# Performance work log

Hardware: AMD Instinct MI355X
Metric: run time of the kernel (lower is better)

The kernel has to match this reference:

```python
import jax, jax.numpy as jnp
import numpy as np

H = 4096
W = 4096
C = 3
OUT = 1024
MAX_MIP = 8  # matches init max_mip_level; mip chain is levels 0..MAX_MIP


def setup_inputs() -> dict:
    key = jax.random.key(0)
    k1, k2, k3 = jax.random.split(key, 3)
    data = jax.random.uniform(k1, (1, H, W, C), dtype=jnp.float32)
    texc = jax.random.uniform(k2, (1, OUT, OUT, 2), dtype=jnp.float32)
    # small UV derivatives -> per-pixel texel footprint of a few texels, so the
    # LOD spans several mip levels (exercises cross-level paged gathers)
    texc_deriv = jax.random.normal(k3, (1, OUT, OUT, 4), dtype=jnp.float32) * 2e-3
    return {"data": data, "texc": texc, "texc_deriv": texc_deriv}


def _avg_pool2(x):
    # 2x2 box-filter mipmap reduction, matching virtual_texture_mipmap_fwd
    b, h, w, c = x.shape
    return x.reshape(b, h // 2, 2, w // 2, 2, c).mean(axis=(2, 4))


def _bilinear_wrap(tex, texc):
    # tex: [1,h,w,c]; texc: [1,Ho,Wo,2] in [0,1); boundary_mode='wrap'
    h, w = tex.shape[1], tex.shape[2]
    x = texc[..., 0] * w - 0.5
    y = texc[..., 1] * h - 0.5
    x0f = jnp.floor(x)
    y0f = jnp.floor(y)
    fx = (x - x0f)[..., None]
    fy = (y - y0f)[..., None]
    x0 = x0f.astype(jnp.int32) % w
    y0 = y0f.astype(jnp.int32) % h
    x1 = (x0 + 1) % w
    y1 = (y0 + 1) % h
    t = tex[0]  # [h,w,c]
    top = t[y0, x0] * (1.0 - fx) + t[y0, x1] * fx
    bot = t[y1, x0] * (1.0 - fx) + t[y1, x1] * fx
    return top * (1.0 - fy) + bot * fy  # [1,Ho,Wo,c]


def _forward(data, texc, texc_deriv):
    # LOD from screen-space UV derivatives (nvdiffrast linear-mipmap-linear)
    dudx = texc_deriv[..., 0] * W
    dvdx = texc_deriv[..., 1] * H
    dudy = texc_deriv[..., 2] * W
    dvdy = texc_deriv[..., 3] * H
    rho2 = jnp.maximum(dudx * dudx + dvdx * dvdx, dudy * dudy + dvdy * dvdy)
    lod = 0.5 * jnp.log2(jnp.maximum(rho2, 1e-20))
    lod = jnp.clip(lod, 0.0, float(MAX_MIP))  # [1,Ho,Wo]

    # build mip pyramid (gradients flow back to base texture, matching
    # virtual_texture_mipmap_bwd accumulation)
    mips = [data]
    for _ in range(MAX_MIP):
        mips.append(_avg_pool2(mips[-1]))

    # trilinear: per-level weight w_l = clip(1 - |lod - l|, 0, 1)
    out = jnp.zeros(texc.shape[:-1] + (C,), dtype=data.dtype)
    for lvl in range(MAX_MIP + 1):
        w_l = jnp.clip(1.0 - jnp.abs(lod - float(lvl)), 0.0, 1.0)[..., None]
        out = out + w_l * _bilinear_wrap(mips[lvl], texc)
    return out


def reference(data, texc, texc_deriv):
    return _forward(data, texc, texc_deriv)
```

## Files before the change

kernel.cpp:

```cpp
#include <hip/hip_runtime.h>
#include <hip/hip_bf16.h>


#define OUT_N (1024 * 1024)

__device__ __forceinline__ unsigned mip_off_b(int lvl) {
    return (67108864u - (67108864u >> (2 * lvl - 2))) / 3u;
}
#define OFF6 22347776u

__device__ __forceinline__ unsigned pack10(float r, float g, float b) {
    unsigned ur = __float2uint_rn(r * 1023.0f);
    unsigned ug = __float2uint_rn(g * 1023.0f);
    unsigned ub = __float2uint_rn(b * 1023.0f);
    return ur | (ug << 10) | (ub << 20);
}

__device__ __forceinline__ void dec_acc(unsigned q, float w, float& r, float& g, float& b) {
    const float s = 1.0f / 1023.0f;
    r = fmaf((float)(q & 1023u) * s, w, r);
    g = fmaf((float)((q >> 10) & 1023u) * s, w, g);
    b = fmaf((float)((q >> 20) & 1023u) * s, w, b);
}

__device__ __forceinline__ float4 dec4(unsigned q) {
    const float s = 1.0f / 1023.0f;
    return float4{(float)(q & 1023u) * s, (float)((q >> 10) & 1023u) * s,
                  (float)((q >> 20) & 1023u) * s, 0.0f};
}

__device__ __forceinline__ float4 avg4(float4 a, float4 b, float4 c, float4 d) {
    return float4{(a.x + b.x + c.x + d.x) * 0.25f,
                  (a.y + b.y + c.y + d.y) * 0.25f,
                  (a.z + b.z + c.z + d.z) * 0.25f, 0.0f};
}

__device__ __forceinline__ void store_quad(char* p, float4 t00, float4 t01,
                                           float4 t10, float4 t11) {
    *(uint4*)p = make_uint4(pack10(t00.x, t00.y, t00.z), pack10(t01.x, t01.y, t01.z),
                            pack10(t10.x, t10.y, t10.z), pack10(t11.x, t11.y, t11.z));
}

__global__ __launch_bounds__(256) void mip_fused(const float* __restrict__ data,
                                                 char* __restrict__ wsb) {
    __shared__ float4 s1[32][33];
    __shared__ float4 s2[16][17];
    __shared__ float4 s3[8][9];
    __shared__ float4 s4[4][5];

    const int t = threadIdx.x;
    const int bx = blockIdx.x & 63;
    const int by = blockIdx.x >> 6;

    {
        int qx = t & 15, qy = t >> 4;
        int r0 = (by << 6) + (qy << 2);
        int c0 = (bx << 6) + (qx << 2);
        const float* p = data + ((size_t)r0 * 4096 + c0) * 3;
        float4 t00 = {0, 0, 0, 0}, t01 = {0, 0, 0, 0};
        float4 t10 = {0, 0, 0, 0}, t11 = {0, 0, 0, 0};
#pragma unroll
        for (int i = 0; i < 4; ++i) {
            const float4* rp = (const float4*)(p + (size_t)i * 4096 * 3);
            float4 A = rp[0], B = rp[1], C = rp[2];
            float ex = A.x + A.w, ey = A.y + B.x, ez = A.z + B.y;
            float fx_ = B.z + C.y, fy_ = B.w + C.z, fz_ = C.x + C.w;
            if (i < 2) {
                t00.x += ex; t00.y += ey; t00.z += ez;
                t01.x += fx_; t01.y += fy_; t01.z += fz_;
            } else {
                t10.x += ex; t10.y += ey; t10.z += ez;
                t11.x += fx_; t11.y += fy_; t11.z += fz_;
            }
        }
        t00.x *= 0.25f; t00.y *= 0.25f; t00.z *= 0.25f;
        t01.x *= 0.25f; t01.y *= 0.25f; t01.z *= 0.25f;
        t10.x *= 0.25f; t10.y *= 0.25f; t10.z *= 0.25f;
        t11.x *= 0.25f; t11.y *= 0.25f; t11.z *= 0.25f;
        s1[2 * qy][2 * qx] = t00;     s1[2 * qy][2 * qx + 1] = t01;
        s1[2 * qy + 1][2 * qx] = t10; s1[2 * qy + 1][2 * qx + 1] = t11;
    }
    __syncthreads();

    if (t < 64) {
        int qx = t & 7, qy = t >> 3;
        int sy = qy << 2, sx = qx << 2;
        float4 t00 = avg4(s1[sy][sx], s1[sy][sx + 1], s1[sy + 1][sx], s1[sy + 1][sx + 1]);
        float4 t01 = avg4(s1[sy][sx + 2], s1[sy][sx + 3], s1[sy + 1][sx + 2], s1[sy + 1][sx + 3]);
        float4 t10 = avg4(s1[sy + 2][sx], s1[sy + 2][sx + 1], s1[sy + 3][sx], s1[sy + 3][sx + 1]);
        float4 t11 = avg4(s1[sy + 2][sx + 2], s1[sy + 2][sx + 3], s1[sy + 3][sx + 2], s1[sy + 3][sx + 3]);
        s2[2 * qy][2 * qx] = t00;     s2[2 * qy][2 * qx + 1] = t01;
        s2[2 * qy + 1][2 * qx] = t10; s2[2 * qy + 1][2 * qx + 1] = t11;
        unsigned gq = ((by << 3) + qy) * 512 + (bx << 3) + qx;
        store_quad(wsb + 16777216u + ((size_t)gq << 4), t00, t01, t10, t11);
    }
    __syncthreads();

    if (t < 16) {
        int qx = t & 3, qy = t >> 2;
        int sy = qy << 2, sx = qx << 2;
        float4 t00 = avg4(s2[sy][sx], s2[sy][sx + 1], s2[sy + 1][sx], s2[sy + 1][sx + 1]);
        float4 t01 = avg4(s2[sy][sx + 2], s2[sy][sx + 3], s2[sy + 1][sx + 2], s2[sy + 1][sx + 3]);
        float4 t10 = avg4(s2[sy + 2][sx], s2[sy + 2][sx + 1], s2[sy + 3][sx], s2[sy + 3][sx + 1]);
        float4 t11 = avg4(s2[sy + 2][sx + 2], s2[sy + 2][sx + 3], s2[sy + 3][sx + 2], s2[sy + 3][sx + 3]);
        s3[2 * qy][2 * qx] = t00;     s3[2 * qy][2 * qx + 1] = t01;
        s3[2 * qy + 1][2 * qx] = t10; s3[2 * qy + 1][2 * qx + 1] = t11;
        unsigned gq = ((by << 2) + qy) * 256 + (bx << 2) + qx;
        store_quad(wsb + 20971520u + ((size_t)gq << 4), t00, t01, t10, t11);
    }
    __syncthreads();

    if (t < 4) {
        int qx = t & 1, qy = t >> 1;
        int sy = qy << 2, sx = qx << 2;
        float4 t00 = avg4(s3[sy][sx], s3[sy][sx + 1], s3[sy + 1][sx], s3[sy + 1][sx + 1]);
        float4 t01 = avg4(s3[sy][sx + 2], s3[sy][sx + 3], s3[sy + 1][sx + 2], s3[sy + 1][sx + 3]);
        float4 t10 = avg4(s3[sy + 2][sx], s3[sy + 2][sx + 1], s3[sy + 3][sx], s3[sy + 3][sx + 1]);
        float4 t11 = avg4(s3[sy + 2][sx + 2], s3[sy + 2][sx + 3], s3[sy + 3][sx + 2], s3[sy + 3][sx + 3]);
        s4[2 * qy][2 * qx] = t00;     s4[2 * qy][2 * qx + 1] = t01;
        s4[2 * qy + 1][2 * qx] = t10; s4[2 * qy + 1][2 * qx + 1] = t11;
        unsigned gq = ((by << 1) + qy) * 128 + (bx << 1) + qx;
        store_quad(wsb + 22020096u + ((size_t)gq << 4), t00, t01, t10, t11);
    }
    __syncthreads();

    if (t == 0) {
        float4 t00 = avg4(s4[0][0], s4[0][1], s4[1][0], s4[1][1]);
        float4 t01 = avg4(s4[0][2], s4[0][3], s4[1][2], s4[1][3]);
        float4 t10 = avg4(s4[2][0], s4[2][1], s4[3][0], s4[3][1]);
        float4 t11 = avg4(s4[2][2], s4[2][3], s4[3][2], s4[3][3]);
        unsigned gq = (unsigned)by * 64u + (unsigned)bx;
        store_quad(wsb + 22282240u + ((size_t)gq << 4), t00, t01, t10, t11);
        float4 l6 = avg4(t00, t01, t10, t11);
        size_t a6 = OFF6 + ((((by >> 1) * 32) + (bx >> 1)) << 4) +
                    ((by & 1) << 3) + ((bx & 1) << 2);
        *(unsigned*)(wsb + a6) = pack10(l6.x, l6.y, l6.z);
    }
}

__device__ __forceinline__ void sample_packed(const char* __restrict__ wsb, int lvl,
                                              float u, float v, float wgt,
                                              float& r, float& g, float& b) {
    int size = 4096 >> lvl;
    float fs = (float)size;
    float x = u * fs - 0.5f;
    float y = v * fs - 0.5f;
    float x0f = floorf(x);
    float y0f = floorf(y);
    float fx = x - x0f;
    float fy = y - y0f;
    int m = size - 1;
    int x0 = ((int)x0f) & m;
    int y0 = ((int)y0f) & m;
    int x1 = (x0 + 1) & m;
    int y1 = (y0 + 1) & m;
    int hs = size >> 1;
    const char* B = wsb + mip_off_b(lvl);
    unsigned q00 = *(const unsigned*)(B + ((((y0 >> 1) * hs) + (x0 >> 1)) << 4) + ((y0 & 1) << 3) + ((x0 & 1) << 2));
    unsigned q01 = *(const unsigned*)(B + ((((y0 >> 1) * hs) + (x1 >> 1)) << 4) + ((y0 & 1) << 3) + ((x1 & 1) << 2));
    unsigned q10 = *(const unsigned*)(B + ((((y1 >> 1) * hs) + (x0 >> 1)) << 4) + ((y1 & 1) << 3) + ((x0 & 1) << 2));
    unsigned q11 = *(const unsigned*)(B + ((((y1 >> 1) * hs) + (x1 >> 1)) << 4) + ((y1 & 1) << 3) + ((x1 & 1) << 2));
    float w00 = (1.0f - fx) * (1.0f - fy) * wgt;
    float w01 = fx * (1.0f - fy) * wgt;
    float w10 = (1.0f - fx) * fy * wgt;
    float w11 = fx * fy * wgt;
    dec_acc(q00, w00, r, g, b);
    dec_acc(q01, w01, r, g, b);
    dec_acc(q10, w10, r, g, b);
    dec_acc(q11, w11, r, g, b);
}

__device__ void sample_fine(const float* __restrict__ data, int lvl,
                            float u, float v, float wgt,
                            float& r, float& g, float& b) {
    int size = 4096 >> lvl;
    float fs = (float)size;
    float x = u * fs - 0.5f;
    float y = v * fs - 0.5f;
    float x0f = floorf(x);
    float y0f = floorf(y);
    float fx = x - x0f;
    float fy = y - y0f;
    int m = size - 1;
    int x0 = ((int)x0f) & m;
    int y0 = ((int)y0f) & m;
    int x1 = (x0 + 1) & m;
    int y1 = (y0 + 1) & m;
    int k = 1 << lvl;
    float inv = wgt / (float)(k * k);
    float ww[2][2] = {{(1.0f - fx) * (1.0f - fy) * inv, fx * (1.0f - fy) * inv},
                      {(1.0f - fx) * fy * inv, fx * fy * inv}};
    int xs[2] = {x0 << lvl, x1 << lvl};
    int ys[2] = {y0 << lvl, y1 << lvl};
    for (int ty = 0; ty < 2; ++ty)
        for (int tx = 0; tx < 2; ++tx) {
            float tr = 0.0f, tg = 0.0f, tb = 0.0f;
            for (int dy = 0; dy < k; ++dy)
                for (int dx = 0; dx < k; ++dx) {
                    const float* p = data + ((size_t)(ys[ty] + dy) * 4096 + xs[tx] + dx) * 3;
                    tr += p[0]; tg += p[1]; tb += p[2];
                }
            r = fmaf(tr, ww[ty][tx], r);
            g = fmaf(tg, ww[ty][tx], g);
            b = fmaf(tb, ww[ty][tx], b);
        }
}

__device__ float4 read_l6(const char* __restrict__ wsb, int xx, int yy) {
    size_t a = OFF6 + ((((yy >> 1) * 32) + (xx >> 1)) << 4) + ((yy & 1) << 3) + ((xx & 1) << 2);
    return dec4(*(const unsigned*)(wsb + a));
}

__device__ void sample_coarse(const char* __restrict__ wsb, int lvl,
                              float u, float v, float wgt,
                              float& r, float& g, float& b) {
    int size = 4096 >> lvl;
    float fs = (float)size;
    float x = u * fs - 0.5f;
    float y = v * fs - 0.5f;
    float x0f = floorf(x);
    float y0f = floorf(y);
    float fx = x - x0f;
    float fy = y - y0f;
    int m = size - 1;
    int x0 = ((int)x0f) & m;
    int y0 = ((int)y0f) & m;
    int x1 = (x0 + 1) & m;
    int y1 = (y0 + 1) & m;
    int s = lvl - 6;
    int k = 1 << s;
    float inv = wgt / (float)(k * k);
    float ww[2][2] = {{(1.0f - fx) * (1.0f - fy) * inv, fx * (1.0f - fy) * inv},
                      {(1.0f - fx) * fy * inv, fx * fy * inv}};
    int xs[2] = {x0 << s, x1 << s};
    int ys[2] = {y0 << s, y1 << s};
    for (int ty = 0; ty < 2; ++ty)
        for (int tx = 0; tx < 2; ++tx) {
            float tr = 0.0f, tg = 0.0f, tb = 0.0f;
            for (int dy = 0; dy < k; ++dy)
                for (int dx = 0; dx < k; ++dx) {
                    float4 c = read_l6(wsb, xs[tx] + dx, ys[ty] + dy);
                    tr += c.x; tg += c.y; tb += c.z;
                }
            r = fmaf(tr, ww[ty][tx], r);
            g = fmaf(tg, ww[ty][tx], g);
            b = fmaf(tb, ww[ty][tx], b);
        }
}

__device__ __forceinline__ void sample_any(const float* __restrict__ data,
                                           const char* __restrict__ wsb, int lvl,
                                           float u, float v, float wgt,
                                           float& r, float& g, float& b) {
    if (lvl >= 2) {
        if (lvl <= 6) sample_packed(wsb, lvl, u, v, wgt, r, g, b);
        else sample_coarse(wsb, lvl, u, v, wgt, r, g, b);
    } else {
        sample_fine(data, lvl, u, v, wgt, r, g, b);
    }
}

__global__ __launch_bounds__(256) void vt_sample(const float* __restrict__ data,
                                                 const char* __restrict__ wsb,
                                                 const float* __restrict__ texc,
                                                 const float* __restrict__ deriv,
                                                 float* __restrict__ out) {
    int p = blockIdx.x * 256 + threadIdx.x;

    float2 uv = ((const float2*)texc)[p];
    float4 dv = ((const float4*)deriv)[p];
    float dudx = dv.x * 4096.0f;
    float dvdx = dv.y * 4096.0f;
    float dudy = dv.z * 4096.0f;
    float dvdy = dv.w * 4096.0f;
    float rho2 = fmaxf(dudx * dudx + dvdx * dvdx, dudy * dudy + dvdy * dvdy);
    float lod = 0.5f * log2f(fmaxf(rho2, 1e-20f));
    lod = fminf(fmaxf(lod, 0.0f), 8.0f);

    int l0 = (int)lod;
    float f = lod - (float)l0;
    int l1 = (l0 < 8) ? (l0 + 1) : 8;

    float r = 0.0f, g = 0.0f, b = 0.0f;
    sample_any(data, wsb, l0, uv.x, uv.y, 1.0f - f, r, g, b);
    sample_any(data, wsb, l1, uv.x, uv.y, f, r, g, b);

    float* o = out + (size_t)p * 3;
    o[0] = r;
    o[1] = g;
    o[2] = b;
}

extern "C" void kernel_launch(void* const* d_in, const int* in_sizes, int n_in,
                              void* d_out, int out_size, void* d_ws, size_t ws_size,
                              hipStream_t stream) {
    const float* data  = (const float*)d_in[0];
    const float* texc  = (const float*)d_in[1];
    const float* deriv = (const float*)d_in[2];
    float* out = (float*)d_out;
    char* wsb  = (char*)d_ws;

    mip_fused<<<4096, 256, 0, stream>>>(data, wsb);
    vt_sample<<<OUT_N / 256, 256, 0, stream>>>(data, wsb, texc, deriv, out);
}
```

Before: 325.7 us.

## Enlarge mip tiles to 128x128 and batch both-level gathers in the sampler

The mip build kernel now processes 128x128 source tiles per block, with each thread reducing an 8x8 patch straight to level 2. This removes the shared-memory level-1 stage, and each block now produces levels 2-6 with a quarter as many blocks. The sampler gets a fast path for packed levels 2-6 that computes addresses for both mip levels and issues all eight gathers before decoding, so more loads are in flight at once. It also switches to fast log2 and fma, and adds launch-bounds occupancy hints. Per-thread register pressure in the mip kernel rises, and far fewer blocks run in parallel.

```diff
diff --git a/kernel.cpp b/kernel.cpp
--- a/kernel.cpp
+++ b/kernel.cpp
@@ -7,6 +7,10 @@
 __device__ __forceinline__ unsigned mip_off_b(int lvl) {
     return (67108864u - (67108864u >> (2 * lvl - 2))) / 3u;
 }
+#define OFF2 16777216u
+#define OFF3 20971520u
+#define OFF4 22020096u
+#define OFF5 22282240u
 #define OFF6 22347776u
 
 __device__ __forceinline__ unsigned pack10(float r, float g, float b) {
@@ -41,63 +45,57 @@
                             pack10(t10.x, t10.y, t10.z), pack10(t11.x, t11.y, t11.z));
 }
 
-__global__ __launch_bounds__(256) void mip_fused(const float* __restrict__ data,
-                                                 char* __restrict__ wsb) {
-    __shared__ float4 s1[32][33];
-    __shared__ float4 s2[16][17];
-    __shared__ float4 s3[8][9];
-    __shared__ float4 s4[4][5];
+__global__ __launch_bounds__(256, 4) void mip_fused(const float* __restrict__ data,
+                                                    char* __restrict__ wsb) {
+    __shared__ float4 s2[32][33];
+    __shared__ float4 s3[16][17];
+    __shared__ float4 s4[8][9];
+    __shared__ float4 s5[4][5];
 
     const int t = threadIdx.x;
-    const int bx = blockIdx.x & 63;
-    const int by = blockIdx.x >> 6;
+    const int bx = blockIdx.x & 31;
+    const int by = blockIdx.x >> 5;
 
     {
         int qx = t & 15, qy = t >> 4;
-        int r0 = (by << 6) + (qy << 2);
-        int c0 = (bx << 6) + (qx << 2);
-        const float* p = data + ((size_t)r0 * 4096 + c0) * 3;
+        int r0 = (by << 7) + (qy << 3);
+        int c0 = (bx << 7) + (qx << 3);
+        const float* p0 = data + ((size_t)r0 * 4096 + c0) * 3;
         float4 t00 = {0, 0, 0, 0}, t01 = {0, 0, 0, 0};
         float4 t10 = {0, 0, 0, 0}, t11 = {0, 0, 0, 0};
 #pragma unroll
-        for (int i = 0; i < 4; ++i) {
-            const float4* rp = (const float4*)(p + (size_t)i * 4096 * 3);
-            float4 A = rp[0], B = rp[1], C = rp[2];
-            float ex = A.x + A.w, ey = A.y + B.x, ez = A.z + B.y;
-            float fx_ = B.z + C.y, fy_ = B.w + C.z, fz_ = C.x + C.w;
-            if (i < 2) {
-                t00.x += ex; t00.y += ey; t00.z += ez;
-                t01.x += fx_; t01.y += fy_; t01.z += fz_;
+        for (int i = 0; i < 8; ++i) {
+            const float4* rp = (const float4*)(p0 + (size_t)i * (4096 * 3));
+            float4 A = rp[0], Bv = rp[1], Cv = rp[2];
+            float4 D = rp[3], E = rp[4], F = rp[5];
+            float lx = A.x + A.w + Bv.z + Cv.y;
+            float ly = A.y + Bv.x + Bv.w + Cv.z;
+            float lz = A.z + Bv.y + Cv.x + Cv.w;
+            float rx = D.x + D.w + E.z + F.y;
+            float ry = D.y + E.x + E.w + F.z;
+            float rz = D.z + E.y + F.x + F.w;
+            if (i < 4) {
+                t00.x += lx; t00.y += ly; t00.z += lz;
+                t01.x += rx; t01.y += ry; t01.z += rz;
             } else {
-                t10.x += ex; t10.y += ey; t10.z += ez;
-                t11.x += fx_; t11.y += fy_; t11.z += fz_;
+                t10.x += lx; t10.y += ly; t10.z += lz;
+                t11.x += rx; t11.y += ry; t11.z += rz;
             }
         }
-        t00.x *= 0.25f; t00.y *= 0.25f; t00.z *= 0.25f;
-        t01.x *= 0.25f; t01.y *= 0.25f; t01.z *= 0.25f;
-        t10.x *= 0.25f; t10.y *= 0.25f; t10.z *= 0.25f;
-        t11.x *= 0.25f; t11.y *= 0.25f; t11.z *= 0.25f;
-        s1[2 * qy][2 * qx] = t00;     s1[2 * qy][2 * qx + 1] = t01;
-        s1[2 * qy + 1][2 * qx] = t10; s1[2 * qy + 1][2 * qx + 1] = t11;
+        const float sc = 1.0f / 16.0f;
+        t00.x *= sc; t00.y *= sc; t00.z *= sc;
+        t01.x *= sc; t01.y *= sc; t01.z *= sc;
+        t10.x *= sc; t10.y *= sc; t10.z *= sc;
+        t11.x *= sc; t11.y *= sc; t11.z *= sc;
+        s2[2 * qy][2 * qx] = t00;     s2[2 * qy][2 * qx + 1] = t01;
+        s2[2 * qy + 1][2 * qx] = t10; s2[2 * qy + 1][2 * qx + 1] = t11;
+        unsigned gq = ((by << 4) + qy) * 512u + (bx << 4) + qx;
+        store_quad(wsb + OFF2 + ((size_t)gq << 4), t00, t01, t10, t11);
     }
     __syncthreads();
 
     if (t < 64) {
         int qx = t & 7, qy = t >> 3;
-        int sy = qy << 2, sx = qx << 2;
-        float4 t00 = avg4(s1[sy][sx], s1[sy][sx + 1], s1[sy + 1][sx], s1[sy + 1][sx + 1]);
-        float4 t01 = avg4(s1[sy][sx + 2], s1[sy][sx + 3], s1[sy + 1][sx + 2], s1[sy + 1][sx + 3]);
-        float4 t10 = avg4(s1[sy + 2][sx], s1[sy + 2][sx + 1], s1[sy + 3][sx], s1[sy + 3][sx + 1]);
-        float4 t11 = avg4(s1[sy + 2][sx + 2], s1[sy + 2][sx + 3], s1[sy + 3][sx + 2], s1[sy + 3][sx + 3]);
-        s2[2 * qy][2 * qx] = t00;     s2[2 * qy][2 * qx + 1] = t01;
-        s2[2 * qy + 1][2 * qx] = t10; s2[2 * qy + 1][2 * qx + 1] = t11;
-        unsigned gq = ((by << 3) + qy) * 512 + (bx << 3) + qx;
-        store_quad(wsb + 16777216u + ((size_t)gq << 4), t00, t01, t10, t11);
-    }
-    __syncthreads();
-
-    if (t < 16) {
-        int qx = t & 3, qy = t >> 2;
         int sy = qy << 2, sx = qx << 2;
         float4 t00 = avg4(s2[sy][sx], s2[sy][sx + 1], s2[sy + 1][sx], s2[sy + 1][sx + 1]);
         float4 t01 = avg4(s2[sy][sx + 2], s2[sy][sx + 3], s2[sy + 1][sx + 2], s2[sy + 1][sx + 3]);
@@ -105,13 +103,13 @@
         float4 t11 = avg4(s2[sy + 2][sx + 2], s2[sy + 2][sx + 3], s2[sy + 3][sx + 2], s2[sy + 3][sx + 3]);
         s3[2 * qy][2 * qx] = t00;     s3[2 * qy][2 * qx + 1] = t01;
         s3[2 * qy + 1][2 * qx] = t10; s3[2 * qy + 1][2 * qx + 1] = t11;
-        unsigned gq = ((by << 2) + qy) * 256 + (bx << 2) + qx;
-        store_quad(wsb + 20971520u + ((size_t)gq << 4), t00, t01, t10, t11);
+        unsigned gq = ((by << 3) + qy) * 256u + (bx << 3) + qx;
+        store_quad(wsb + OFF3 + ((size_t)gq << 4), t00, t01, t10, t11);
     }
     __syncthreads();
 
-    if (t < 4) {
-        int qx = t & 1, qy = t >> 1;
+    if (t < 16) {
+        int qx = t & 3, qy = t >> 2;
         int sy = qy << 2, sx = qx << 2;
         float4 t00 = avg4(s3[sy][sx], s3[sy][sx + 1], s3[sy + 1][sx], s3[sy + 1][sx + 1]);
         float4 t01 = avg4(s3[sy][sx + 2], s3[sy][sx + 3], s3[sy + 1][sx + 2], s3[sy + 1][sx + 3]);
@@ -119,55 +117,79 @@
         float4 t11 = avg4(s3[sy + 2][sx + 2], s3[sy + 2][sx + 3], s3[sy + 3][sx + 2], s3[sy + 3][sx + 3]);
         s4[2 * qy][2 * qx] = t00;     s4[2 * qy][2 * qx + 1] = t01;
         s4[2 * qy + 1][2 * qx] = t10; s4[2 * qy + 1][2 * qx + 1] = t11;
-        unsigned gq = ((by << 1) + qy) * 128 + (bx << 1) + qx;
-        store_quad(wsb + 22020096u + ((size_t)gq << 4), t00, t01, t10, t11);
+        unsigned gq = ((by << 2) + qy) * 128u + (bx << 2) + qx;
+        store_quad(wsb + OFF4 + ((size_t)gq << 4), t00, t01, t10, t11);
     }
     __syncthreads();
 
+    if (t < 4) {
+        int qx = t & 1, qy = t >> 1;
+        int sy = qy << 2, sx = qx << 2;
+        float4 t00 = avg4(s4[sy][sx], s4[sy][sx + 1], s4[sy + 1][sx], s4[sy + 1][sx + 1]);
+        float4 t01 = avg4(s4[sy][sx + 2], s4[sy][sx + 3], s4[sy + 1][sx + 2], s4[sy + 1][sx + 3]);
+        float4 t10 = avg4(s4[sy + 2][sx], s4[sy + 2][sx + 1], s4[sy + 3][sx], s4[sy + 3][sx + 1]);
+        float4 t11 = avg4(s4[sy + 2][sx + 2], s4[sy + 2][sx + 3], s4[sy + 3][sx + 2], s4[sy + 3][sx + 3]);
+        s5[2 * qy][2 * qx] = t00;     s5[2 * qy][2 * qx + 1] = t01;
+        s5[2 * qy + 1][2 * qx] = t10; s5[2 * qy + 1][2 * qx + 1] = t11;
+        unsigned gq = ((by << 1) + qy) * 64u + (bx << 1) + qx;
+        store_quad(wsb + OFF5 + ((size_t)gq << 4), t00, t01, t10, t11);
+    }
+    __syncthreads();
+
     if (t == 0) {
-        float4 t00 = avg4(s4[0][0], s4[0][1], s4[1][0], s4[1][1]);
-        float4 t01 = avg4(s4[0][2], s4[0][3], s4[1][2], s4[1][3]);
-        float4 t10 = avg4(s4[2][0], s4[2][1], s4[3][0], s4[3][1]);
-        float4 t11 = avg4(s4[2][2], s4[2][3], s4[3][2], s4[3][3]);
-        unsigned gq = (unsigned)by * 64u + (unsigned)bx;
-        store_quad(wsb + 22282240u + ((size_t)gq << 4), t00, t01, t10, t11);
-        float4 l6 = avg4(t00, t01, t10, t11);
-        size_t a6 = OFF6 + ((((by >> 1) * 32) + (bx >> 1)) << 4) +
-                    ((by & 1) << 3) + ((bx & 1) << 2);
-        *(unsigned*)(wsb + a6) = pack10(l6.x, l6.y, l6.z);
-    }
-}
-
-__device__ __forceinline__ void sample_packed(const char* __restrict__ wsb, int lvl,
-                                              float u, float v, float wgt,
-                                              float& r, float& g, float& b) {
+        float4 t00 = avg4(s5[0][0], s5[0][1], s5[1][0], s5[1][1]);
+        float4 t01 = avg4(s5[0][2], s5[0][3], s5[1][2], s5[1][3]);
+        float4 t10 = avg4(s5[2][0], s5[2][1], s5[3][0], s5[3][1]);
+        float4 t11 = avg4(s5[2][2], s5[2][3], s5[3][2], s5[3][3]);
+        unsigned gq = (unsigned)by * 32u + (unsigned)bx;
+        store_quad(wsb + OFF6 + ((size_t)gq << 4), t00, t01, t10, t11);
+    }
+}
+
+__device__ __forceinline__ void tap_off(int lvl, float u, float v,
+                                        unsigned& o00, unsigned& o01,
+                                        unsigned& o10, unsigned& o11,
+                                        float& fx, float& fy) {
     int size = 4096 >> lvl;
     float fs = (float)size;
-    float x = u * fs - 0.5f;
-    float y = v * fs - 0.5f;
+    float x = fmaf(u, fs, -0.5f);
+    float y = fmaf(v, fs, -0.5f);
     float x0f = floorf(x);
     float y0f = floorf(y);
-    float fx = x - x0f;
-    float fy = y - y0f;
+    fx = x - x0f;
+    fy = y - y0f;
     int m = size - 1;
     int x0 = ((int)x0f) & m;
     int y0 = ((int)y0f) & m;
     int x1 = (x0 + 1) & m;
     int y1 = (y0 + 1) & m;
     int hs = size >> 1;
+    unsigned r0 = (unsigned)((y0 >> 1) * hs);
+    unsigned r1 = (unsigned)((y1 >> 1) * hs);
+    unsigned c0 = (unsigned)(x0 >> 1), c1 = (unsigned)(x1 >> 1);
+    unsigned sy0 = (unsigned)((y0 & 1) << 3), sy1 = (unsigned)((y1 & 1) << 3);
+    unsigned sx0 = (unsigned)((x0 & 1) << 2), sx1 = (unsigned)((x1 & 1) << 2);
+    o00 = ((r0 + c0) << 4) + sy0 + sx0;
+    o01 = ((r0 + c1) << 4) + sy0 + sx1;
+    o10 = ((r1 + c0) << 4) + sy1 + sx0;
+    o11 = ((r1 + c1) << 4) + sy1 + sx1;
+}
+
+__device__ __forceinline__ void sample_packed(const char* __restrict__ wsb, int lvl,
+                                              float u, float v, float wgt,
+                                              float& r, float& g, float& b) {
+    unsigned o00, o01, o10, o11;
+    float fx, fy;
+    tap_off(lvl, u, v, o00, o01, o10, o11, fx, fy);
     const char* B = wsb + mip_off_b(lvl);
-    unsigned q00 = *(const unsigned*)(B + ((((y0 >> 1) * hs) + (x0 >> 1)) << 4) + ((y0 & 1) << 3) + ((x0 & 1) << 2));
-    unsigned q01 = *(const unsigned*)(B + ((((y0 >> 1) * hs) + (x1 >> 1)) << 4) + ((y0 & 1) << 3) + ((x1 & 1) << 2));
-    unsigned q10 = *(const unsigned*)(B + ((((y1 >> 1) * hs) + (x0 >> 1)) << 4) + ((y1 & 1) << 3) + ((x0 & 1) << 2));
-    unsigned q11 = *(const unsigned*)(B + ((((y1 >> 1) * hs) + (x1 >> 1)) << 4) + ((y1 & 1) << 3) + ((x1 & 1) << 2));
-    float w00 = (1.0f - fx) * (1.0f - fy) * wgt;
-    float w01 = fx * (1.0f - fy) * wgt;
-    float w10 = (1.0f - fx) * fy * wgt;
-    float w11 = fx * fy * wgt;
-    dec_acc(q00, w00, r, g, b);
-    dec_acc(q01, w01, r, g, b);
-    dec_acc(q10, w10, r, g, b);
-    dec_acc(q11, w11, r, g, b);
+    unsigned q00 = *(const unsigned*)(B + o00);
+    unsigned q01 = *(const unsigned*)(B + o01);
+    unsigned q10 = *(const unsigned*)(B + o10);
+    unsigned q11 = *(const unsigned*)(B + o11);
+    dec_acc(q00, (1.0f - fx) * (1.0f - fy) * wgt, r, g, b);
+    dec_acc(q01, fx * (1.0f - fy) * wgt, r, g, b);
+    dec_acc(q10, (1.0f - fx) * fy * wgt, r, g, b);
+    dec_acc(q11, fx * fy * wgt, r, g, b);
 }
 
 __device__ void sample_fine(const float* __restrict__ data, int lvl,
@@ -260,11 +282,11 @@
     }
 }
 
-__global__ __launch_bounds__(256) void vt_sample(const float* __restrict__ data,
-                                                 const char* __restrict__ wsb,
-                                                 const float* __restrict__ texc,
-                                                 const float* __restrict__ deriv,
-                                                 float* __restrict__ out) {
+__global__ __launch_bounds__(256, 4) void vt_sample(const float* __restrict__ data,
+                                                    const char* __restrict__ wsb,
+                                                    const float* __restrict__ texc,
+                                                    const float* __restrict__ deriv,
+                                                    float* __restrict__ out) {
     int p = blockIdx.x * 256 + threadIdx.x;
 
     float2 uv = ((const float2*)texc)[p];
@@ -273,8 +295,8 @@
     float dvdx = dv.y * 4096.0f;
     float dudy = dv.z * 4096.0f;
     float dvdy = dv.w * 4096.0f;
-    float rho2 = fmaxf(dudx * dudx + dvdx * dvdx, dudy * dudy + dvdy * dvdy);
-    float lod = 0.5f * log2f(fmaxf(rho2, 1e-20f));
+    float rho2 = fmaxf(fmaf(dudx, dudx, dvdx * dvdx), fmaf(dudy, dudy, dvdy * dvdy));
+    float lod = 0.5f * __log2f(fmaxf(rho2, 1e-20f));
     lod = fminf(fmaxf(lod, 0.0f), 8.0f);
 
     int l0 = (int)lod;
@@ -282,8 +304,35 @@
     int l1 = (l0 < 8) ? (l0 + 1) : 8;
 
     float r = 0.0f, g = 0.0f, b = 0.0f;
-    sample_any(data, wsb, l0, uv.x, uv.y, 1.0f - f, r, g, b);
-    sample_any(data, wsb, l1, uv.x, uv.y, f, r, g, b);
+
+    if (__builtin_expect((unsigned)(l0 - 2) <= 3u, 1)) {
+        unsigned a00, a01, a10, a11, b00, b01, b10, b11;
+        float fx0, fy0, fx1, fy1;
+        const char* B0 = wsb + mip_off_b(l0);
+        const char* B1 = wsb + mip_off_b(l1);
+        tap_off(l0, uv.x, uv.y, a00, a01, a10, a11, fx0, fy0);
+        tap_off(l1, uv.x, uv.y, b00, b01, b10, b11, fx1, fy1);
+        unsigned q0 = *(const unsigned*)(B0 + a00);
+        unsigned q1 = *(const unsigned*)(B0 + a01);
+        unsigned q2 = *(const unsigned*)(B0 + a10);
+        unsigned q3 = *(const unsigned*)(B0 + a11);
+        unsigned q4 = *(const unsigned*)(B1 + b00);
+        unsigned q5 = *(const unsigned*)(B1 + b01);
+        unsigned q6 = *(const unsigned*)(B1 + b10);
+        unsigned q7 = *(const unsigned*)(B1 + b11);
+        float w0 = 1.0f - f;
+        dec_acc(q0, (1.0f - fx0) * (1.0f - fy0) * w0, r, g, b);
+        dec_acc(q1, fx0 * (1.0f - fy0) * w0, r, g, b);
+        dec_acc(q2, (1.0f - fx0) * fy0 * w0, r, g, b);
+        dec_acc(q3, fx0 * fy0 * w0, r, g, b);
+        dec_acc(q4, (1.0f - fx1) * (1.0f - fy1) * f, r, g, b);
+        dec_acc(q5, fx1 * (1.0f - fy1) * f, r, g, b);
+        dec_acc(q6, (1.0f - fx1) * fy1 * f, r, g, b);
+        dec_acc(q7, fx1 * fy1 * f, r, g, b);
+    } else {
+        sample_any(data, wsb, l0, uv.x, uv.y, 1.0f - f, r, g, b);
+        sample_any(data, wsb, l1, uv.x, uv.y, f, r, g, b);
+    }
 
     float* o = out + (size_t)p * 3;
     o[0] = r;
@@ -300,6 +349,6 @@
     float* out = (float*)d_out;
     char* wsb  = (char*)d_ws;
 
-    mip_fused<<<4096, 256, 0, stream>>>(data, wsb);
+    mip_fused<<<1024, 256, 0, stream>>>(data, wsb);
     vt_sample<<<OUT_N / 256, 256, 0, stream>>>(data, wsb, texc, deriv, out);
 }
```

After: 369.1 us. +13.3%, slower.
